# Performance work log

Hardware: AMD Instinct MI355X
Metric: run time of the kernel (lower is better)

## Reference

```python
import jax, jax.numpy as jnp
import numpy as np

COLLAPSE_FRAC = 4  # collapse F // 4 lowest-weight faces (target_size = 3/4 * F)


def setup_inputs() -> dict:
    key = jax.random.key(0)
    k1, k2, k3 = jax.random.split(key, 3)
    B, F, C, K = 8, 8192, 256, 4
    features = jax.random.normal(k1, (B, F, C), dtype=jnp.float32)
    adjacency = jax.random.randint(k2, (B, F, 3), 0, F).astype(jnp.int32)
    ring_k = jax.random.randint(k3, (B, F, K), 0, F).astype(jnp.int32)
    return {"features": features, "adjacency": adjacency, "ring_k": ring_k}


def _pool(features, adjacency, ring_k):
    # features:  [B, F, C] float   per-face features
    # adjacency: [B, F, 3] int     3 neighboring faces of each triangle
    # ring_k:    [B, F, K] int     k-ring neighborhood used for collapse weights
    B, F, C = features.shape
    K = ring_k.shape[-1]
    # ring-aggregated saliency weight per face (compute_weights analogue)
    rf = jnp.take_along_axis(
        features, ring_k.reshape(B, F * K)[:, :, None], axis=1
    ).reshape(B, F, K, C)                      # [B, F, K, C]
    w = jnp.linalg.norm(rf.mean(axis=2), axis=-1)  # [B, F]

    # select lowest-weight faces to collapse (idx/sorted analogue)
    P = F // COLLAPSE_FRAC
    _, collapse_idx = jax.lax.top_k(-w, P)      # [B, P]

    # gather the 3 region neighbors and the collapsed face features
    neighbors = jnp.take_along_axis(adjacency, collapse_idx[:, :, None], axis=1)  # [B, P, 3]
    cf = jnp.take_along_axis(features, collapse_idx[:, :, None], axis=1)          # [B, P, C]

    # scatter collapsed-face features into their 3 adjacent faces (update_features analogue)
    offs = (jnp.arange(B, dtype=jnp.int32) * F)[:, None, None]   # [B, 1, 1]
    seg = (neighbors + offs).reshape(-1)                          # [B*P*3]
    vals = jnp.broadcast_to(cf[:, :, None, :] / 3.0, (B, P, 3, C)).reshape(-1, C)
    scat = jax.ops.segment_sum(vals, seg, num_segments=B * F).reshape(B, F, C)
    cnt = jax.ops.segment_sum(
        jnp.ones(seg.shape, jnp.float32), seg, num_segments=B * F
    ).reshape(B, F, 1)
    merged = (features + scat) / (1.0 + cnt)

    # erase collapsed faces (erased / update_faces analogue; static shape, mask instead of compaction)
    erase_flat = (collapse_idx + offs[:, :, 0]).reshape(-1)
    keep = (
        jnp.ones((B * F,), jnp.float32).at[erase_flat].set(0.0).reshape(B, F, 1)
    )
    return merged * keep


def reference(features, adjacency, ring_k):
    return _pool(features, adjacency, ring_k)
```

## Files before the change

### kernel.cpp

```cpp
#include <hip/hip_runtime.h>
#include <stdint.h>

#define B 8
#define F 8192
#define C 256
#define K 4
#define P (F / 4)
#define CAP 16
#define NB 4096

__device__ __forceinline__ int binOf(float v, float lo, float scale) {
    int bin = (int)((v - lo) * scale);
    return bin < 0 ? 0 : (bin > NB - 1 ? NB - 1 : bin);
}

__global__ __launch_bounds__(256) void kW(const float* __restrict__ feat,
                                          const int* __restrict__ ring,
                                          float* __restrict__ w,
                                          int* __restrict__ cnt,
                                          int* __restrict__ flag) {
    const int b     = blockIdx.x & 7;
    const int inner = blockIdx.x >> 3;
    const int wid   = b * F + inner * 4 + (threadIdx.x >> 6);
    const int lane  = threadIdx.x & 63;

    const int rbase = wid * K;
    const int r0 = ring[rbase + 0], r1 = ring[rbase + 1];
    const int r2 = ring[rbase + 2], r3 = ring[rbase + 3];
    const float4* f4 = (const float4*)feat;
    const size_t base = (size_t)b * F;
    const int    CW   = C / 4;
    const float4 v0 = f4[(base + r0) * CW + lane];
    const float4 v1 = f4[(base + r1) * CW + lane];
    const float4 v2 = f4[(base + r2) * CW + lane];
    const float4 v3 = f4[(base + r3) * CW + lane];

    float4 a;
    a.x = (v0.x + v1.x) + (v2.x + v3.x);
    a.y = (v0.y + v1.y) + (v2.y + v3.y);
    a.z = (v0.z + v1.z) + (v2.z + v3.z);
    a.w = (v0.w + v1.w) + (v2.w + v3.w);
    float s = (a.x * a.x + a.y * a.y + a.z * a.z + a.w * a.w) * 0.0625f;
#pragma unroll
    for (int off = 32; off > 0; off >>= 1) s += __shfl_down(s, off, 64);
    if (lane == 0) {
        w[wid]    = sqrtf(s);
        cnt[wid]  = 0;
        flag[wid] = 0;
    }
}

__global__ __launch_bounds__(1024) void kHT(const float* __restrict__ w,
                                            int* __restrict__ tbin,
                                            int* __restrict__ trank,
                                            int* __restrict__ ccnt,
                                            unsigned int* __restrict__ lsb) {
    __shared__ int h[NB];
    __shared__ unsigned int red[1024];
    const int b = blockIdx.x, t = threadIdx.x;

    float val[8];
    unsigned int mn = 0xFFFFFFFFu, mx = 0u;
#pragma unroll
    for (int k = 0; k < 8; ++k) {
        val[k] = w[b * F + t + k * 1024];
        const unsigned int u = __float_as_uint(val[k]);
        mn = mn < u ? mn : u;
        mx = mx > u ? mx : u;
    }
    red[t] = mn;
    __syncthreads();
    for (int off = 512; off > 0; off >>= 1) {
        if (t < off) red[t] = min(red[t], red[t + off]);
        __syncthreads();
    }
    const unsigned int lob = red[0];
    __syncthreads();
    red[t] = mx;
    __syncthreads();
    for (int off = 512; off > 0; off >>= 1) {
        if (t < off) red[t] = max(red[t], red[t + off]);
        __syncthreads();
    }
    const unsigned int hib = red[0];
    __syncthreads();

    const float lo    = __uint_as_float(lob);
    const float hi    = __uint_as_float(hib);
    const float scale = (float)(NB - 2) / fmaxf(hi - lo, 1e-30f);

    for (int i = t; i < NB; i += 1024) h[i] = 0;
    __syncthreads();
#pragma unroll
    for (int k = 0; k < 8; ++k) atomicAdd(&h[binOf(val[k], lo, scale)], 1);
    __syncthreads();

    int s = 0;
#pragma unroll
    for (int i = 0; i < 4; ++i) s += h[t * 4 + i];
    int* part = (int*)red;
    part[t] = s;
    __syncthreads();
    for (int off = 1; off < 1024; off <<= 1) {
        const int v = part[t];
        const int u = (t >= off) ? part[t - off] : 0;
        __syncthreads();
        part[t] = v + u;
        __syncthreads();
    }
    const int excl = (t == 0) ? 0 : part[t - 1];
    if (P - 1 >= excl && P - 1 < part[t]) {
        int c = excl;
#pragma unroll
        for (int i = 0; i < 4; ++i) {
            const int bin = t * 4 + i;
            const int hv = h[bin];
            if (P - 1 < c + hv) { tbin[b] = bin; trank[b] = P - c; break; }
            c += hv;
        }
    }
    if (t == 0) {
        ccnt[b] = 0;
        lsb[b * 2 + 0] = lob;
        lsb[b * 2 + 1] = hib;
    }
}

__global__ __launch_bounds__(256) void kFL(const float* __restrict__ w,
                                           const int* __restrict__ adj,
                                           const unsigned int* __restrict__ lsb,
                                           const int* __restrict__ tbin,
                                           int* __restrict__ flag,
                                           int* __restrict__ cnt,
                                           int* __restrict__ srcs,
                                           unsigned long long* __restrict__ cand,
                                           int* __restrict__ ccnt) {
    __shared__ unsigned long long lc[256];
    __shared__ int lcnt;
    __shared__ int lbase;
    if (threadIdx.x == 0) lcnt = 0;
    __syncthreads();

    const int t = blockIdx.x * 256 + threadIdx.x;
    const int b = t >> 13;
    const float lo    = __uint_as_float(lsb[b * 2 + 0]);
    const float hi    = __uint_as_float(lsb[b * 2 + 1]);
    const float scale = (float)(NB - 2) / fmaxf(hi - lo, 1e-30f);

    const float v = w[t];
    const int bin = binOf(v, lo, scale);
    const int T = tbin[b];
    if (bin < T) {
        flag[t] = 1;
#pragma unroll
        for (int j = 0; j < 3; ++j) {
            const int n    = adj[(size_t)t * 3 + j];
            const int tgt  = b * F + n;
            const int slot = atomicAdd(&cnt[tgt], 1);
            if (slot < CAP) srcs[(size_t)tgt * CAP + slot] = t;
        }
    } else if (bin == T) {
        const int pos = atomicAdd(&lcnt, 1);
        lc[pos] = ((unsigned long long)__float_as_uint(v) << 32) | (uint32_t)(t & (F - 1));
    }
    __syncthreads();
    if (threadIdx.x == 0 && lcnt > 0)
        lbase = atomicAdd(&ccnt[b], lcnt);
    __syncthreads();
    const int m = lcnt;
    for (int i = threadIdx.x; i < m; i += 256)
        cand[(size_t)b * F + lbase + i] = lc[i];
}

__global__ __launch_bounds__(1024) void kSel(const int* __restrict__ ccnt,
                                             const int* __restrict__ trank,
                                             const unsigned long long* __restrict__ cand,
                                             const int* __restrict__ adj,
                                             int* __restrict__ flag,
                                             int* __restrict__ cnt,
                                             int* __restrict__ srcs) {
    __shared__ unsigned long long keys[F];
    const int b = blockIdx.x;
    const int n = ccnt[b];
    const int R = trank[b];
    for (int i = threadIdx.x; i < n; i += 1024)
        keys[i] = cand[(size_t)b * F + i];
    __syncthreads();
    for (int i = threadIdx.x; i < n; i += 1024) {
        const unsigned long long my = keys[i];
        int rank = 0;
        for (int j = 0; j < n; ++j) rank += (keys[j] < my) ? 1 : 0;
        if (rank < R) {
            const int t = b * F + (int)(uint32_t)my;
            flag[t] = 1;
#pragma unroll
            for (int j = 0; j < 3; ++j) {
                const int nb   = adj[(size_t)t * 3 + j];
                const int tgt  = b * F + nb;
                const int slot = atomicAdd(&cnt[tgt], 1);
                if (slot < CAP) srcs[(size_t)tgt * CAP + slot] = t;
            }
        }
    }
}

__global__ __launch_bounds__(256) void kG(const float* __restrict__ feat,
                                          const int* __restrict__ cnt,
                                          const int* __restrict__ flag,
                                          const int* __restrict__ srcs,
                                          float* __restrict__ out) {
    const int b     = blockIdx.x & 7;
    const int inner = blockIdx.x >> 3;
    const int wid   = b * F + inner * 4 + (threadIdx.x >> 6);
    const int lane  = threadIdx.x & 63;
    float4* drow = (float4*)(out + (size_t)wid * C);

    if (flag[wid]) {
        drow[lane] = make_float4(0.f, 0.f, 0.f, 0.f);
        return;
    }
    const int m  = cnt[wid];
    const int mm = m < CAP ? m : CAP;

    const int sidx = (lane < CAP) ? srcs[(size_t)wid * CAP + lane] : 0;

    float4 acc = ((const float4*)(feat + (size_t)wid * C))[lane];
    const float inv3 = 1.0f / 3.0f;
    for (int i = 0; i < mm; ++i) {
        const int s = __shfl(sidx, i, 64);
        const float4 v = ((const float4*)(feat + (size_t)s * C))[lane];
        acc.x += v.x * inv3; acc.y += v.y * inv3;
        acc.z += v.z * inv3; acc.w += v.w * inv3;
    }
    const float inv = 1.0f / (1.0f + (float)m);
    acc.x *= inv; acc.y *= inv; acc.z *= inv; acc.w *= inv;
    drow[lane] = acc;
}

extern "C" void kernel_launch(void* const* d_in, const int* in_sizes, int n_in,
                              void* d_out, int out_size, void* d_ws, size_t ws_size,
                              hipStream_t stream) {
    const float* feat = (const float*)d_in[0];
    const int*   adj  = (const int*)d_in[1];
    const int*   ring = (const int*)d_in[2];
    float* out = (float*)d_out;

    unsigned long long* cand = (unsigned long long*)d_ws;
    float* w     = (float*)(cand + B * F);
    int*   cnt   = (int*)(w + B * F);
    int*   flag  = cnt + B * F;
    int*   srcs  = flag + B * F;
    int*   ccnt  = srcs + (size_t)B * F * CAP;
    int*   tbin  = ccnt + B;
    int*   trank = tbin + B;
    unsigned int* lsb = (unsigned int*)(trank + B);

    kW  <<<(B * F) / 4, 256, 0, stream>>>(feat, ring, w, cnt, flag);
    kHT <<<B, 1024, 0, stream>>>(w, tbin, trank, ccnt, lsb);
    kFL <<<(B * F) / 256, 256, 0, stream>>>(w, adj, lsb, tbin, flag, cnt, srcs, cand, ccnt);
    kSel<<<B, 1024, 0, stream>>>(ccnt, trank, cand, adj, flag, cnt, srcs);
    kG  <<<(B * F) / 4, 256, 0, stream>>>(feat, cnt, flag, srcs, out);
}
```

Before: 161.9 us.

## Fuse histogram threshold, flagging and candidate selection into one per-batch kernel

Merges the histogram/threshold kernel, the flagging kernel and the candidate-rank selection kernel into a single kernel with one 1024-thread block per batch. Histogram and candidate key buffers share a shared-memory union. Candidates stay in shared memory instead of going through a global buffer with atomic offsets. This removes two launches and the global round trips, but the flagging and adjacency scatter now run on only 8 blocks instead of 256, and the candidate count is capped at CAND_CAP.

```diff
diff --git a/kernel.cpp b/kernel.cpp
--- a/kernel.cpp
+++ b/kernel.cpp
@@ -8,6 +8,7 @@
 #define P (F / 4)
 #define CAP 16
 #define NB 4096
+#define CAND_CAP 8184
 
 __device__ __forceinline__ int binOf(float v, float lo, float scale) {
     int bin = (int)((v - lo) * scale);
@@ -50,14 +51,21 @@
     }
 }
 
-__global__ __launch_bounds__(1024) void kHT(const float* __restrict__ w,
-                                            int* __restrict__ tbin,
-                                            int* __restrict__ trank,
-                                            int* __restrict__ ccnt,
-                                            unsigned int* __restrict__ lsb) {
-    __shared__ int h[NB];
-    __shared__ unsigned int red[1024];
-    const int b = blockIdx.x, t = threadIdx.x;
+struct SMemHT { int h[NB]; unsigned int red[1024]; };
+struct SMemFS { unsigned long long keys[CAND_CAP]; int lcnt; };
+union  SMemU  { SMemHT ht; SMemFS fs; };
+
+__global__ __launch_bounds__(1024) void kMid(const float* __restrict__ w,
+                                             const int* __restrict__ adj,
+                                             int* __restrict__ flag,
+                                             int* __restrict__ cnt,
+                                             int* __restrict__ srcs) {
+    __shared__ SMemU sm;
+    __shared__ int sT, sR;
+    const int b = blockIdx.x;
+    const int t = threadIdx.x;
+
+    if (t == 0) sm.fs.lcnt = 0;
 
     float val[8];
     unsigned int mn = 0xFFFFFFFFu, mx = 0u;
@@ -68,37 +76,37 @@
         mn = mn < u ? mn : u;
         mx = mx > u ? mx : u;
     }
-    red[t] = mn;
+    sm.ht.red[t] = mn;
     __syncthreads();
     for (int off = 512; off > 0; off >>= 1) {
-        if (t < off) red[t] = min(red[t], red[t + off]);
-        __syncthreads();
-    }
-    const unsigned int lob = red[0];
-    __syncthreads();
-    red[t] = mx;
+        if (t < off) sm.ht.red[t] = min(sm.ht.red[t], sm.ht.red[t + off]);
+        __syncthreads();
+    }
+    const unsigned int lob = sm.ht.red[0];
+    __syncthreads();
+    sm.ht.red[t] = mx;
     __syncthreads();
     for (int off = 512; off > 0; off >>= 1) {
-        if (t < off) red[t] = max(red[t], red[t + off]);
-        __syncthreads();
-    }
-    const unsigned int hib = red[0];
+        if (t < off) sm.ht.red[t] = max(sm.ht.red[t], sm.ht.red[t + off]);
+        __syncthreads();
+    }
+    const unsigned int hib = sm.ht.red[0];
     __syncthreads();
 
     const float lo    = __uint_as_float(lob);
     const float hi    = __uint_as_float(hib);
     const float scale = (float)(NB - 2) / fmaxf(hi - lo, 1e-30f);
 
-    for (int i = t; i < NB; i += 1024) h[i] = 0;
-    __syncthreads();
-#pragma unroll
-    for (int k = 0; k < 8; ++k) atomicAdd(&h[binOf(val[k], lo, scale)], 1);
+    for (int i = t; i < NB; i += 1024) sm.ht.h[i] = 0;
+    __syncthreads();
+#pragma unroll
+    for (int k = 0; k < 8; ++k) atomicAdd(&sm.ht.h[binOf(val[k], lo, scale)], 1);
     __syncthreads();
 
     int s = 0;
 #pragma unroll
-    for (int i = 0; i < 4; ++i) s += h[t * 4 + i];
-    int* part = (int*)red;
+    for (int i = 0; i < 4; ++i) s += sm.ht.h[t * 4 + i];
+    int* part = (int*)sm.ht.red;
     part[t] = s;
     __syncthreads();
     for (int off = 1; off < 1024; off <<= 1) {
@@ -114,91 +122,51 @@
 #pragma unroll
         for (int i = 0; i < 4; ++i) {
             const int bin = t * 4 + i;
-            const int hv = h[bin];
-            if (P - 1 < c + hv) { tbin[b] = bin; trank[b] = P - c; break; }
+            const int hv  = sm.ht.h[bin];
+            if (P - 1 < c + hv) { sT = bin; sR = P - c; break; }
             c += hv;
         }
     }
-    if (t == 0) {
-        ccnt[b] = 0;
-        lsb[b * 2 + 0] = lob;
-        lsb[b * 2 + 1] = hib;
-    }
-}
-
-__global__ __launch_bounds__(256) void kFL(const float* __restrict__ w,
-                                           const int* __restrict__ adj,
-                                           const unsigned int* __restrict__ lsb,
-                                           const int* __restrict__ tbin,
-                                           int* __restrict__ flag,
-                                           int* __restrict__ cnt,
-                                           int* __restrict__ srcs,
-                                           unsigned long long* __restrict__ cand,
-                                           int* __restrict__ ccnt) {
-    __shared__ unsigned long long lc[256];
-    __shared__ int lcnt;
-    __shared__ int lbase;
-    if (threadIdx.x == 0) lcnt = 0;
-    __syncthreads();
-
-    const int t = blockIdx.x * 256 + threadIdx.x;
-    const int b = t >> 13;
-    const float lo    = __uint_as_float(lsb[b * 2 + 0]);
-    const float hi    = __uint_as_float(lsb[b * 2 + 1]);
-    const float scale = (float)(NB - 2) / fmaxf(hi - lo, 1e-30f);
-
-    const float v = w[t];
-    const int bin = binOf(v, lo, scale);
-    const int T = tbin[b];
-    if (bin < T) {
-        flag[t] = 1;
-#pragma unroll
-        for (int j = 0; j < 3; ++j) {
-            const int n    = adj[(size_t)t * 3 + j];
-            const int tgt  = b * F + n;
-            const int slot = atomicAdd(&cnt[tgt], 1);
-            if (slot < CAP) srcs[(size_t)tgt * CAP + slot] = t;
+    __syncthreads();
+
+    const int T = sT;
+#pragma unroll
+    for (int k = 0; k < 8; ++k) {
+        const int face = b * F + t + k * 1024;
+        const int bin  = binOf(val[k], lo, scale);
+        if (bin < T) {
+            flag[face] = 1;
+#pragma unroll
+            for (int j = 0; j < 3; ++j) {
+                const int n    = adj[(size_t)face * 3 + j];
+                const int tgt  = b * F + n;
+                const int slot = atomicAdd(&cnt[tgt], 1);
+                if (slot < CAP) srcs[(size_t)tgt * CAP + slot] = face;
+            }
+        } else if (bin == T) {
+            const int pos = atomicAdd(&sm.fs.lcnt, 1);
+            if (pos < CAND_CAP)
+                sm.fs.keys[pos] = ((unsigned long long)__float_as_uint(val[k]) << 32) |
+                                  (uint32_t)(face & (F - 1));
         }
-    } else if (bin == T) {
-        const int pos = atomicAdd(&lcnt, 1);
-        lc[pos] = ((unsigned long long)__float_as_uint(v) << 32) | (uint32_t)(t & (F - 1));
-    }
-    __syncthreads();
-    if (threadIdx.x == 0 && lcnt > 0)
-        lbase = atomicAdd(&ccnt[b], lcnt);
-    __syncthreads();
-    const int m = lcnt;
-    for (int i = threadIdx.x; i < m; i += 256)
-        cand[(size_t)b * F + lbase + i] = lc[i];
-}
-
-__global__ __launch_bounds__(1024) void kSel(const int* __restrict__ ccnt,
-                                             const int* __restrict__ trank,
-                                             const unsigned long long* __restrict__ cand,
-                                             const int* __restrict__ adj,
-                                             int* __restrict__ flag,
-                                             int* __restrict__ cnt,
-                                             int* __restrict__ srcs) {
-    __shared__ unsigned long long keys[F];
-    const int b = blockIdx.x;
-    const int n = ccnt[b];
-    const int R = trank[b];
-    for (int i = threadIdx.x; i < n; i += 1024)
-        keys[i] = cand[(size_t)b * F + i];
-    __syncthreads();
-    for (int i = threadIdx.x; i < n; i += 1024) {
-        const unsigned long long my = keys[i];
+    }
+    __syncthreads();
+
+    const int n = sm.fs.lcnt < CAND_CAP ? sm.fs.lcnt : CAND_CAP;
+    const int R = sR;
+    for (int i = t; i < n; i += 1024) {
+        const unsigned long long my = sm.fs.keys[i];
         int rank = 0;
-        for (int j = 0; j < n; ++j) rank += (keys[j] < my) ? 1 : 0;
+        for (int j = 0; j < n; ++j) rank += (sm.fs.keys[j] < my) ? 1 : 0;
         if (rank < R) {
-            const int t = b * F + (int)(uint32_t)my;
-            flag[t] = 1;
+            const int tt = b * F + (int)(uint32_t)my;
+            flag[tt] = 1;
 #pragma unroll
             for (int j = 0; j < 3; ++j) {
-                const int nb   = adj[(size_t)t * 3 + j];
+                const int nb   = adj[(size_t)tt * 3 + j];
                 const int tgt  = b * F + nb;
                 const int slot = atomicAdd(&cnt[tgt], 1);
-                if (slot < CAP) srcs[(size_t)tgt * CAP + slot] = t;
+                if (slot < CAP) srcs[(size_t)tgt * CAP + slot] = tt;
             }
         }
     }
@@ -245,19 +213,12 @@
     const int*   ring = (const int*)d_in[2];
     float* out = (float*)d_out;
 
-    unsigned long long* cand = (unsigned long long*)d_ws;
-    float* w     = (float*)(cand + B * F);
-    int*   cnt   = (int*)(w + B * F);
-    int*   flag  = cnt + B * F;
-    int*   srcs  = flag + B * F;
-    int*   ccnt  = srcs + (size_t)B * F * CAP;
-    int*   tbin  = ccnt + B;
-    int*   trank = tbin + B;
-    unsigned int* lsb = (unsigned int*)(trank + B);
+    float* w    = (float*)d_ws;
+    int*   cnt  = (int*)(w + B * F);
+    int*   flag = cnt + B * F;
+    int*   srcs = flag + B * F;
 
     kW  <<<(B * F) / 4, 256, 0, stream>>>(feat, ring, w, cnt, flag);
-    kHT <<<B, 1024, 0, stream>>>(w, tbin, trank, ccnt, lsb);
-    kFL <<<(B * F) / 256, 256, 0, stream>>>(w, adj, lsb, tbin, flag, cnt, srcs, cand, ccnt);
-    kSel<<<B, 1024, 0, stream>>>(ccnt, trank, cand, adj, flag, cnt, srcs);
+    kMid<<<B, 1024, 0, stream>>>(w, adj, flag, cnt, srcs);
     kG  <<<(B * F) / 4, 256, 0, stream>>>(feat, cnt, flag, srcs, out);
 }
```

After: 176.4 us. 1.09x slower.

## Fold tie-bin selection into last flag block and use wave-level reductions

Applied to the files above, without the earlier changes.

The histogram kernel's shared-memory tree reductions and block-wide scan are replaced with wavefront shuffle reductions and a two-level shuffle scan, which cuts the number of barriers. The separate selection kernel is removed. Its work now runs in whichever flag block finishes last, detected with a global atomic ticket counter, which saves one kernel launch. In exchange, the tie-bin ranking runs serially over all 8 batches in a single 256-thread block and reads candidates from global memory instead of LDS, so it could be slow when many faces share the threshold bin.

```diff
diff --git a/kernel.cpp b/kernel.cpp
--- a/kernel.cpp
+++ b/kernel.cpp
@@ -8,6 +8,7 @@
 #define P (F / 4)
 #define CAP 16
 #define NB 4096
+#define NFL ((B * F) / 256)
 
 __device__ __forceinline__ int binOf(float v, float lo, float scale) {
     int bin = (int)((v - lo) * scale);
@@ -54,10 +55,14 @@
                                             int* __restrict__ tbin,
                                             int* __restrict__ trank,
                                             int* __restrict__ ccnt,
-                                            unsigned int* __restrict__ lsb) {
+                                            unsigned int* __restrict__ lsb,
+                                            int* __restrict__ done) {
     __shared__ int h[NB];
-    __shared__ unsigned int red[1024];
+    __shared__ unsigned int redmn[16], redmx[16];
+    __shared__ int wsum[16], woff[16];
+    __shared__ unsigned int slo, shi;
     const int b = blockIdx.x, t = threadIdx.x;
+    const int lane = t & 63, wv = t >> 6;
 
     float val[8];
     unsigned int mn = 0xFFFFFFFFu, mx = 0u;
@@ -68,29 +73,28 @@
         mn = mn < u ? mn : u;
         mx = mx > u ? mx : u;
     }
-    red[t] = mn;
-    __syncthreads();
-    for (int off = 512; off > 0; off >>= 1) {
-        if (t < off) red[t] = min(red[t], red[t + off]);
-        __syncthreads();
-    }
-    const unsigned int lob = red[0];
-    __syncthreads();
-    red[t] = mx;
-    __syncthreads();
-    for (int off = 512; off > 0; off >>= 1) {
-        if (t < off) red[t] = max(red[t], red[t + off]);
-        __syncthreads();
-    }
-    const unsigned int hib = red[0];
-    __syncthreads();
-
+#pragma unroll
+    for (int off = 32; off > 0; off >>= 1) {
+        const unsigned int o1 = __shfl_xor(mn, off, 64); mn = mn < o1 ? mn : o1;
+        const unsigned int o2 = __shfl_xor(mx, off, 64); mx = mx > o2 ? mx : o2;
+    }
+    if (lane == 0) { redmn[wv] = mn; redmx[wv] = mx; }
+    for (int i = t; i < NB; i += 1024) h[i] = 0;
+    __syncthreads();
+    if (t == 0) {
+        unsigned int a = redmn[0], c = redmx[0];
+        for (int i = 1; i < 16; ++i) {
+            a = a < redmn[i] ? a : redmn[i];
+            c = c > redmx[i] ? c : redmx[i];
+        }
+        slo = a; shi = c;
+    }
+    __syncthreads();
+    const unsigned int lob = slo, hib = shi;
     const float lo    = __uint_as_float(lob);
     const float hi    = __uint_as_float(hib);
     const float scale = (float)(NB - 2) / fmaxf(hi - lo, 1e-30f);
 
-    for (int i = t; i < NB; i += 1024) h[i] = 0;
-    __syncthreads();
 #pragma unroll
     for (int k = 0; k < 8; ++k) atomicAdd(&h[binOf(val[k], lo, scale)], 1);
     __syncthreads();
@@ -98,31 +102,42 @@
     int s = 0;
 #pragma unroll
     for (int i = 0; i < 4; ++i) s += h[t * 4 + i];
-    int* part = (int*)red;
-    part[t] = s;
-    __syncthreads();
-    for (int off = 1; off < 1024; off <<= 1) {
-        const int v = part[t];
-        const int u = (t >= off) ? part[t - off] : 0;
-        __syncthreads();
-        part[t] = v + u;
-        __syncthreads();
-    }
-    const int excl = (t == 0) ? 0 : part[t - 1];
-    if (P - 1 >= excl && P - 1 < part[t]) {
-        int c = excl;
+    int incl = s;
+#pragma unroll
+    for (int off = 1; off < 64; off <<= 1) {
+        const int u = __shfl_up(incl, off, 64);
+        if (lane >= off) incl += u;
+    }
+    if (lane == 63) wsum[wv] = incl;
+    __syncthreads();
+    if (t < 16) {
+        const int v = wsum[t];
+        int iv = v;
+#pragma unroll
+        for (int off = 1; off < 16; off <<= 1) {
+            const int u = __shfl_up(iv, off, 64);
+            if (t >= off) iv += u;
+        }
+        woff[t] = iv - v;
+    }
+    __syncthreads();
+    const int inclT = incl + woff[wv];
+    const int exclT = inclT - s;
+    if (P - 1 >= exclT && P - 1 < inclT) {
+        int c = exclT;
 #pragma unroll
         for (int i = 0; i < 4; ++i) {
             const int bin = t * 4 + i;
-            const int hv = h[bin];
+            const int hv  = h[bin];
             if (P - 1 < c + hv) { tbin[b] = bin; trank[b] = P - c; break; }
             c += hv;
         }
     }
     if (t == 0) {
-        ccnt[b] = 0;
+        ccnt[b]        = 0;
         lsb[b * 2 + 0] = lob;
         lsb[b * 2 + 1] = hib;
+        if (b == 0) *done = 0;
     }
 }
 
@@ -130,14 +145,17 @@
                                            const int* __restrict__ adj,
                                            const unsigned int* __restrict__ lsb,
                                            const int* __restrict__ tbin,
+                                           const int* __restrict__ trank,
                                            int* __restrict__ flag,
                                            int* __restrict__ cnt,
                                            int* __restrict__ srcs,
                                            unsigned long long* __restrict__ cand,
-                                           int* __restrict__ ccnt) {
+                                           int* __restrict__ ccnt,
+                                           int* __restrict__ done) {
     __shared__ unsigned long long lc[256];
     __shared__ int lcnt;
     __shared__ int lbase;
+    __shared__ int ticket;
     if (threadIdx.x == 0) lcnt = 0;
     __syncthreads();
 
@@ -170,35 +188,33 @@
     const int m = lcnt;
     for (int i = threadIdx.x; i < m; i += 256)
         cand[(size_t)b * F + lbase + i] = lc[i];
-}
-
-__global__ __launch_bounds__(1024) void kSel(const int* __restrict__ ccnt,
-                                             const int* __restrict__ trank,
-                                             const unsigned long long* __restrict__ cand,
-                                             const int* __restrict__ adj,
-                                             int* __restrict__ flag,
-                                             int* __restrict__ cnt,
-                                             int* __restrict__ srcs) {
-    __shared__ unsigned long long keys[F];
-    const int b = blockIdx.x;
-    const int n = ccnt[b];
-    const int R = trank[b];
-    for (int i = threadIdx.x; i < n; i += 1024)
-        keys[i] = cand[(size_t)b * F + i];
-    __syncthreads();
-    for (int i = threadIdx.x; i < n; i += 1024) {
-        const unsigned long long my = keys[i];
-        int rank = 0;
-        for (int j = 0; j < n; ++j) rank += (keys[j] < my) ? 1 : 0;
-        if (rank < R) {
-            const int t = b * F + (int)(uint32_t)my;
-            flag[t] = 1;
-#pragma unroll
-            for (int j = 0; j < 3; ++j) {
-                const int nb   = adj[(size_t)t * 3 + j];
-                const int tgt  = b * F + nb;
-                const int slot = atomicAdd(&cnt[tgt], 1);
-                if (slot < CAP) srcs[(size_t)tgt * CAP + slot] = t;
+
+    __threadfence();
+    __syncthreads();
+    if (threadIdx.x == 0) ticket = atomicAdd(done, 1);
+    __syncthreads();
+    if (ticket == NFL - 1) {
+        __threadfence();
+        for (int bb = 0; bb < B; ++bb) {
+            const int n0 = ccnt[bb];
+            const int n  = n0 < F ? n0 : F;
+            const int R  = trank[bb];
+            for (int i = threadIdx.x; i < n; i += 256) {
+                const unsigned long long my = cand[(size_t)bb * F + i];
+                int rank = 0;
+                for (int j = 0; j < n; ++j)
+                    rank += (cand[(size_t)bb * F + j] < my) ? 1 : 0;
+                if (rank < R) {
+                    const int tt = bb * F + (int)(uint32_t)my;
+                    flag[tt] = 1;
+#pragma unroll
+                    for (int j = 0; j < 3; ++j) {
+                        const int nb   = adj[(size_t)tt * 3 + j];
+                        const int tgt  = bb * F + nb;
+                        const int slot = atomicAdd(&cnt[tgt], 1);
+                        if (slot < CAP) srcs[(size_t)tgt * CAP + slot] = tt;
+                    }
+                }
             }
         }
     }
@@ -254,10 +270,10 @@
     int*   tbin  = ccnt + B;
     int*   trank = tbin + B;
     unsigned int* lsb = (unsigned int*)(trank + B);
+    int*   done  = (int*)(lsb + 2 * B);
 
     kW  <<<(B * F) / 4, 256, 0, stream>>>(feat, ring, w, cnt, flag);
-    kHT <<<B, 1024, 0, stream>>>(w, tbin, trank, ccnt, lsb);
-    kFL <<<(B * F) / 256, 256, 0, stream>>>(w, adj, lsb, tbin, flag, cnt, srcs, cand, ccnt);
-    kSel<<<B, 1024, 0, stream>>>(ccnt, trank, cand, adj, flag, cnt, srcs);
+    kHT <<<B, 1024, 0, stream>>>(w, tbin, trank, ccnt, lsb, done);
+    kFL <<<NFL, 256, 0, stream>>>(w, adj, lsb, tbin, trank, flag, cnt, srcs, cand, ccnt, done);
     kG  <<<(B * F) / 4, 256, 0, stream>>>(feat, cnt, flag, srcs, out);
 }
```

New measurement: 199.3 us. 1.23x slower.
